# Optimization experiments

Hardware: AMD Instinct MI355X
Metric: run time of the kernel (lower is better)

## Reference

```python
import jax, jax.numpy as jnp
import numpy as np
from jax import lax

DIM = 512
NUM_HEADS = 8
RANK = 4
SR = 2
LN_EPS = 1e-5


def setup_inputs() -> dict:
    key = jax.random.key(0)
    ks = jax.random.split(key, 16)
    B, N, C = 8, 1024, DIM
    H = W = 32
    r = C // RANK  # 128 low-rank bottleneck
    std = 0.02
    x = jax.random.normal(ks[0], (B, N, C), dtype=jnp.float32)
    # training-path random mask: rand > sparsity(=0.5), True = masked out
    mask = jax.random.bernoulli(ks[1], 0.5, (B, NUM_HEADS, N, (H // SR) * (W // SR)))
    # low-rank QKV projection weights, torch Linear layout (out, in), no bias
    q_w1 = jax.random.normal(ks[2], (r, C), dtype=jnp.float32) * std
    q_w2 = jax.random.normal(ks[3], (C, r), dtype=jnp.float32) * std
    k_w1 = jax.random.normal(ks[4], (r, C), dtype=jnp.float32) * std
    k_w2 = jax.random.normal(ks[5], (C, r), dtype=jnp.float32) * std
    v_w1 = jax.random.normal(ks[6], (r, C), dtype=jnp.float32) * std
    v_w2 = jax.random.normal(ks[7], (C, r), dtype=jnp.float32) * std
    # depthwise sr conv: torch Conv2d(dim, dim, k=SR, stride=SR, groups=dim) -> (C,1,SR,SR)
    fan_out = SR * SR * C // C  # = SR*SR
    sr_w = jax.random.normal(ks[8], (C, 1, SR, SR), dtype=jnp.float32) * np.sqrt(2.0 / fan_out)
    sr_b = jnp.zeros((C,), dtype=jnp.float32)
    ln_g = jnp.ones((C,), dtype=jnp.float32)
    ln_b = jnp.zeros((C,), dtype=jnp.float32)
    proj_w = jax.random.normal(ks[9], (C, C), dtype=jnp.float32) * std
    proj_b = jnp.zeros((C,), dtype=jnp.float32)
    return {"x": x, "mask": mask, "q_w1": q_w1, "q_w2": q_w2, "k_w1": k_w1,
            "k_w2": k_w2, "v_w1": v_w1, "v_w2": v_w2, "sr_w": sr_w, "sr_b": sr_b,
            "ln_g": ln_g, "ln_b": ln_b, "proj_w": proj_w, "proj_b": proj_b,
            "H": H, "W": W}


def reference(x, mask, q_w1, q_w2, k_w1, k_w2, v_w1, v_w2, sr_w, sr_b,
              ln_g, ln_b, proj_w, proj_b, H, W):
    B, N, C = x.shape
    hd = C // NUM_HEADS
    scale = hd ** -0.5
    # low-rank q projection
    q = (x @ q_w1.T) @ q_w2.T  # (B,N,C)
    q = q.reshape(B, N, NUM_HEADS, hd).transpose(0, 2, 1, 3)  # (B,h,N,d)
    # spatial reduction: depthwise conv k=stride=SR, then LayerNorm
    x_ = x.transpose(0, 2, 1).reshape(B, C, H, W)
    x_ = lax.conv_general_dilated(x_, sr_w, (SR, SR), 'VALID',
                                  feature_group_count=C,
                                  dimension_numbers=('NCHW', 'OIHW', 'NCHW'))
    x_ = x_ + sr_b[None, :, None, None]
    x_ = x_.reshape(B, C, -1).transpose(0, 2, 1)  # (B, N_new, C)
    mu = jnp.mean(x_, axis=-1, keepdims=True)
    var = jnp.mean(jnp.square(x_ - mu), axis=-1, keepdims=True)
    x_ = (x_ - mu) / jnp.sqrt(var + LN_EPS) * ln_g + ln_b
    Nn = x_.shape[1]
    k = ((x_ @ k_w1.T) @ k_w2.T).reshape(B, Nn, NUM_HEADS, hd).transpose(0, 2, 1, 3)
    v = ((x_ @ v_w1.T) @ v_w2.T).reshape(B, Nn, NUM_HEADS, hd).transpose(0, 2, 1, 3)
    # masked scaled dot-product attention (training path: random mask -> -inf)
    attn = jnp.einsum('bhnd,bhmd->bhnm', q, k) * scale
    attn = jnp.where(mask, -jnp.inf, attn)
    attn = jax.nn.softmax(attn, axis=-1)
    out = jnp.einsum('bhnm,bhmd->bhnd', attn, v)  # (B,h,N,d)
    out = out.transpose(0, 2, 1, 3).reshape(B, N, C)
    out = out @ proj_w.T + proj_b
    return out
```

## Files before the change

kernel.cpp:

```cpp
#include <hip/hip_runtime.h>
#include <hip/hip_bf16.h>
#include <math.h>
#include <stdint.h>

#define DIMC   512
#define NHEAD  8
#define HD     64
#define NTOK   1024
#define MTOK   256
#define BSZ    8
#define LN_EPS 1e-5f

typedef __attribute__((ext_vector_type(8))) short  short8v;
typedef __attribute__((ext_vector_type(4))) float  f32x4;
typedef __attribute__((ext_vector_type(4))) unsigned short us4;

typedef const __attribute__((address_space(1))) unsigned int* gas1_t;
typedef __attribute__((address_space(3))) unsigned int*       las3_t;

__device__ __forceinline__ void gload_lds16(const void* g, void* l) {
    __builtin_amdgcn_global_load_lds((gas1_t)g, (las3_t)l, 16, 0, 0);
}

__device__ __forceinline__ unsigned short f2bf(float f) {
    union { float f; unsigned int u; } v; v.f = f;
    unsigned int u = v.u;
    return (unsigned short)((u + 0x7FFFu + ((u >> 16) & 1u)) >> 16);
}

__global__ void detect_mask_kernel(const unsigned int* __restrict__ m,
                                   int* __restrict__ flag)
{
    const int lane = threadIdx.x & 63;
    const unsigned int w = m[lane];
    const unsigned long long not01 = __ballot(w > 1u);
    const unsigned long long notf  = __ballot(w != 0u && w != 0x3F800000u);
    if (lane == 0) *flag = (not01 == 0ull) ? 0 : ((notf == 0ull) ? 2 : 1);
}

__global__ __launch_bounds__(256)
void pack_mask_kernel(const void* __restrict__ maskp, const int* __restrict__ flag,
                      unsigned long long* __restrict__ packed)
{
    const int w = threadIdx.x >> 6, lane = threadIdx.x & 63;
    const long long row = (long long)blockIdx.x * 4 + w;
    const int mtype = *flag;
    int m0, m1, m2, m3;
    if (mtype == 0) {
        const int4 v = ((const int4*)maskp)[row * 64 + lane];
        m0 = v.x; m1 = v.y; m2 = v.z; m3 = v.w;
    } else if (mtype == 1) {
        const uchar4 v = ((const uchar4*)maskp)[row * 64 + lane];
        m0 = v.x; m1 = v.y; m2 = v.z; m3 = v.w;
    } else {
        const float4 v = ((const float4*)maskp)[row * 64 + lane];
        m0 = (v.x != 0.f); m1 = (v.y != 0.f); m2 = (v.z != 0.f); m3 = (v.w != 0.f);
    }
    const unsigned long long b0 = __ballot(m0 != 0);
    const unsigned long long b1 = __ballot(m1 != 0);
    const unsigned long long b2 = __ballot(m2 != 0);
    const unsigned long long b3 = __ballot(m3 != 0);
    if (lane < 4) {
        const unsigned long long v = lane == 0 ? b0 : lane == 1 ? b1
                                   : lane == 2 ? b2 : b3;
        packed[row * 4 + lane] = v;
    }
}

__global__ __launch_bounds__(256)
void f32_to_bf16_kernel(const float* __restrict__ in, unsigned short* __restrict__ out,
                        int n4)
{
    for (int i = blockIdx.x * 256 + threadIdx.x; i < n4; i += gridDim.x * 256) {
        const float4 v = ((const float4*)in)[i];
        us4 p;
        p[0] = f2bf(v.x); p[1] = f2bf(v.y); p[2] = f2bf(v.z); p[3] = f2bf(v.w);
        ((us4*)out)[i] = p;
    }
}

__global__ __launch_bounds__(256)
void convert_weights_kernel(const float* __restrict__ qw1, const float* __restrict__ kw1,
                            const float* __restrict__ vw1, const float* __restrict__ qw2,
                            const float* __restrict__ kw2, const float* __restrict__ vw2,
                            const float* __restrict__ pw,  unsigned short* __restrict__ out,
                            unsigned short* __restrict__ w1t)
{
    const int e = (blockIdx.x * 256 + threadIdx.x) * 4;
    const float* src; int off;
    if      (e < 65536)  { src = qw1; off = e; }
    else if (e < 131072) { src = kw1; off = e - 65536; }
    else if (e < 196608) { src = vw1; off = e - 131072; }
    else if (e < 262144) { src = qw2; off = e - 196608; }
    else if (e < 327680) { src = kw2; off = e - 262144; }
    else if (e < 393216) { src = vw2; off = e - 327680; }
    else                 { src = pw;  off = e - 393216; }
    const float4 v = *(const float4*)(src + off);
    us4 p;
    p[0] = f2bf(v.x); p[1] = f2bf(v.y); p[2] = f2bf(v.z); p[3] = f2bf(v.w);
    *(us4*)(out + e) = p;
    if (e < 196608) {
        const int mat = e >> 16, rem = e & 65535;
        const int k = rem >> 9, j = rem & 511;
#pragma unroll
        for (int t = 0; t < 4; ++t)
            w1t[mat * 65536 + (j + t) * 128 + k] = p[t];
    }
}

template<int OUT_MODE, int BSEL>
__global__ __launch_bounds__(256)
void gemm_bf16(const unsigned short* __restrict__ A,
               const unsigned short* __restrict__ B,
               const float* __restrict__ bias,
               void* __restrict__ Cp, int M, int N, int K)
{
    __shared__ unsigned short As[2][128 * 64];
    __shared__ unsigned short Bs[2][128 * 64];

    const int tid  = threadIdx.x;
    const int w    = tid >> 6;
    const int lane = tid & 63;
    const int c16  = lane & 15;
    const int g    = lane >> 4;
    const int wr   = w >> 1, wc = w & 1;
    const size_t bm = (size_t)blockIdx.y * 128;
    const size_t bn = (size_t)blockIdx.x * 128;
    if (BSEL) B += (bm >> 9) * 65536;

    f32x4 acc[4][4];
#pragma unroll
    for (int i = 0; i < 4; ++i)
#pragma unroll
        for (int j = 0; j < 4; ++j) acc[i][j] = (f32x4){0.f, 0.f, 0.f, 0.f};

    const int NT = K >> 6;

    auto stage = [&](int buf, int kt) {
#pragma unroll
        for (int i = 0; i < 4; ++i) {
            const int o   = (((i * 4 + w) * 64) + lane) * 16;
            const int row = o >> 7;
            const int col = (o & 127) >> 1;
            gload_lds16(A + (bm + row) * K + kt + col, (char*)As[buf] + o);
        }
#pragma unroll
        for (int i = 0; i < 4; ++i) {
            const int o   = (((i * 4 + w) * 64) + lane) * 16;
            const int row = o >> 7;
            const int col = (o & 127) >> 1;
            gload_lds16(B + (bn + row) * K + kt + col, (char*)Bs[buf] + o);
        }
    };

    stage(0, 0);
    int cur = 0;
    for (int t = 0; t < NT; ++t) {
        if (t + 1 < NT) {
            stage(cur ^ 1, (t + 1) * 64);
            asm volatile("s_waitcnt vmcnt(8)" ::: "memory");
        } else {
            asm volatile("s_waitcnt vmcnt(0)" ::: "memory");
        }
        asm volatile("s_barrier" ::: "memory");
#pragma unroll
        for (int kk = 0; kk < 2; ++kk) {
            short8v a[4], bb[4];
#pragma unroll
            for (int mf = 0; mf < 4; ++mf)
                a[mf] = *(const short8v*)(&As[cur][(wr * 64 + mf * 16 + c16) * 64 + kk * 32 + g * 8]);
#pragma unroll
            for (int nf = 0; nf < 4; ++nf)
                bb[nf] = *(const short8v*)(&Bs[cur][(wc * 64 + nf * 16 + c16) * 64 + kk * 32 + g * 8]);
#pragma unroll
            for (int mf = 0; mf < 4; ++mf)
#pragma unroll
                for (int nf = 0; nf < 4; ++nf)
                    acc[mf][nf] = __builtin_amdgcn_mfma_f32_16x16x32_bf16(a[mf], bb[nf], acc[mf][nf], 0, 0, 0);
        }
        asm volatile("s_barrier" ::: "memory");
        cur ^= 1;
    }

#pragma unroll
    for (int mf = 0; mf < 4; ++mf) {
#pragma unroll
        for (int nf = 0; nf < 4; ++nf) {
            const size_t col = bn + wc * 64 + nf * 16 + c16;
            const size_t r0  = bm + wr * 64 + mf * 16 + g * 4;
            if (OUT_MODE == 0) {
                float* C = (float*)Cp;
                const float bv = (bias != nullptr) ? bias[col] : 0.f;
#pragma unroll
                for (int r = 0; r < 4; ++r)
                    C[(r0 + r) * N + col] = acc[mf][nf][r] + bv;
            } else if (OUT_MODE == 1) {
                unsigned short* C = (unsigned short*)Cp;
#pragma unroll
                for (int r = 0; r < 4; ++r)
                    C[(r0 + r) * N + col] = f2bf(acc[mf][nf][r]);
            } else {
                if (col < 512) {
                    unsigned short* Ck = (unsigned short*)Cp;
#pragma unroll
                    for (int r = 0; r < 4; ++r)
                        Ck[(r0 + r) * 512 + col] = f2bf(acc[mf][nf][r]);
                } else {
                    unsigned short* Cv = (unsigned short*)Cp + 1048576;
                    const size_t b  = r0 >> 8;
                    const size_t m0 = r0 & 255;
                    us4 p;
                    p[0] = f2bf(acc[mf][nf][0]); p[1] = f2bf(acc[mf][nf][1]);
                    p[2] = f2bf(acc[mf][nf][2]); p[3] = f2bf(acc[mf][nf][3]);
                    *(us4*)(Cv + (b * 512 + (col - 512)) * 256 + m0) = p;
                }
            }
        }
    }
}

__global__ __launch_bounds__(512)
void conv_ln_kernel(const float* __restrict__ x, const float* __restrict__ srw,
                    const float* __restrict__ srb, const float* __restrict__ lng,
                    const float* __restrict__ lnb, unsigned short* __restrict__ xr)
{
    const int c  = threadIdx.x;
    const int bn = blockIdx.x;
    const int b  = bn >> 8;
    const int np = bn & 255;
    const int ho = np >> 4, wo = np & 15;
    const int n00 = (ho * 2) * 32 + wo * 2;

    const float* xb = x + ((size_t)b * NTOK) * DIMC + c;
    const float4 w = *(const float4*)(srw + c * 4);
    float y = srb[c]
            + xb[(size_t)(n00     ) * DIMC] * w.x
            + xb[(size_t)(n00 + 1 ) * DIMC] * w.y
            + xb[(size_t)(n00 + 32) * DIMC] * w.z
            + xb[(size_t)(n00 + 33) * DIMC] * w.w;

    float s = y, s2 = y * y;
#pragma unroll
    for (int off = 32; off > 0; off >>= 1) {
        s  += __shfl_down(s,  off);
        s2 += __shfl_down(s2, off);
    }
    __shared__ float red[16];
    __shared__ float stats[2];
    const int lane = c & 63, wid = c >> 6;
    if (lane == 0) { red[wid] = s; red[8 + wid] = s2; }
    __syncthreads();
    if (c == 0) {
        float ts = 0.f, ts2 = 0.f;
#pragma unroll
        for (int i = 0; i < 8; ++i) { ts += red[i]; ts2 += red[8 + i]; }
        const float mu  = ts * (1.f / 512.f);
        const float var = ts2 * (1.f / 512.f) - mu * mu;
        stats[0] = mu;
        stats[1] = rsqrtf(var + LN_EPS);
    }
    __syncthreads();
    const float mu = stats[0], rstd = stats[1];
    xr[((size_t)(b * MTOK + np)) * DIMC + c] = f2bf((y - mu) * rstd * lng[c] + lnb[c]);
}

__global__ __launch_bounds__(256, 4)
void attn_mfma(const unsigned short* __restrict__ qb,
               const unsigned short* __restrict__ kb,
               const unsigned short* __restrict__ vt,
               const unsigned long long* __restrict__ pmask,
               unsigned short* __restrict__ ob)
{
    __shared__ unsigned short Ks[16384];

    const int tid  = threadIdx.x;
    const int w    = tid >> 6;
    const int lane = tid & 63;
    const int g    = lane >> 4;
    const int c16  = lane & 15;
    const int bh   = blockIdx.x & 63;
    const int qt   = blockIdx.x >> 6;
    const int b    = bh >> 3;
    const int h    = bh & 7;
    const int q0   = qt * 64 + w * 16;

    const unsigned short* kgb = kb + ((size_t)b * MTOK) * DIMC + h * HD;
#pragma unroll
    for (int t = 0; t < 8; ++t) {
        const int chunk = t * 256 + w * 64 + lane;
        const int o_dma = chunk * 16;
        const int row   = o_dma >> 7;
        const int o_log = o_dma ^ ((row & 7) << 4);
        const int slot  = (o_log >> 4) & 7;
        gload_lds16(kgb + (size_t)row * DIMC + slot * 8, (char*)Ks + o_dma);
    }

    const size_t prow = (size_t)bh * NTOK + q0 + g * 4;
    unsigned mlo[4], mhi[4];
#pragma unroll
    for (int r = 0; r < 4; ++r) {
        const unsigned long long pm = pmask[(prow + r) * 4 + (c16 & 3)] >> (c16 >> 2);
        mlo[r] = (unsigned)pm;
        mhi[r] = (unsigned)(pm >> 32);
    }
    short8v qf[2];
#pragma unroll
    for (int ks = 0; ks < 2; ++ks)
        qf[ks] = *(const short8v*)(qb + ((size_t)(b * NTOK + q0 + c16)) * DIMC
                                      + h * HD + ks * 32 + g * 8);

    asm volatile("s_waitcnt vmcnt(0)" ::: "memory");
    asm volatile("s_barrier" ::: "memory");

    f32x4 s[16];
#pragma unroll
    for (int nf = 0; nf < 16; ++nf) s[nf] = (f32x4){0.f, 0.f, 0.f, 0.f};
#pragma unroll
    for (int nf = 0; nf < 16; ++nf) {
        const int kr = nf * 16 + c16;
        const int sw = (kr & 7) << 4;
#pragma unroll
        for (int ks = 0; ks < 2; ++ks) {
            const int o = (kr << 7) + ks * 64 + g * 16;
            const short8v kf = *(const short8v*)((const char*)Ks + (o ^ sw));
            s[nf] = __builtin_amdgcn_mfma_f32_16x16x32_bf16(qf[ks], kf, s[nf], 0, 0, 0);
        }
    }

    const float scale = 0.125f;
#pragma unroll
    for (int nf = 0; nf < 16; ++nf) {
#pragma unroll
        for (int r = 0; r < 4; ++r) {
            const unsigned bit = ((nf < 8 ? (mlo[r] >> (nf * 4))
                                          : (mhi[r] >> ((nf - 8) * 4))) & 1u);
            s[nf][r] = bit ? -INFINITY : s[nf][r] * scale;
        }
    }

    float mx[4] = {-1e30f, -1e30f, -1e30f, -1e30f};
#pragma unroll
    for (int nf = 0; nf < 16; ++nf)
#pragma unroll
        for (int r = 0; r < 4; ++r) mx[r] = fmaxf(mx[r], s[nf][r]);
#pragma unroll
    for (int off = 8; off >= 1; off >>= 1)
#pragma unroll
        for (int r = 0; r < 4; ++r) mx[r] = fmaxf(mx[r], __shfl_xor(mx[r], off, 64));

    float sm[4] = {0.f, 0.f, 0.f, 0.f};
#pragma unroll
    for (int nf = 0; nf < 16; ++nf)
#pragma unroll
        for (int r = 0; r < 4; ++r) {
            const float p = __expf(s[nf][r] - mx[r]);
            s[nf][r] = p;
            sm[r] += p;
        }
#pragma unroll
    for (int off = 8; off >= 1; off >>= 1)
#pragma unroll
        for (int r = 0; r < 4; ++r) sm[r] += __shfl_xor(sm[r], off, 64);
    float inv[4];
#pragma unroll
    for (int r = 0; r < 4; ++r) inv[r] = 1.0f / sm[r];

    asm volatile("s_barrier" ::: "memory");

    unsigned short* pw = Ks + w * 4096;
#pragma unroll
    for (int nf = 0; nf < 16; ++nf) {
        const int key = nf * 16 + c16;
#pragma unroll
        for (int r = 0; r < 4; ++r) {
            const int row = g * 4 + r;
            pw[row * 256 + (key ^ ((row & 7) << 3))] = f2bf(s[nf][r] * inv[r]);
        }
    }

    f32x4 o[4];
#pragma unroll
    for (int df = 0; df < 4; ++df) o[df] = (f32x4){0.f, 0.f, 0.f, 0.f};

    const int prw = c16;
    const unsigned short* pr = pw + prw * 256;
#pragma unroll
    for (int kf = 0; kf < 8; ++kf) {
        const int k0 = kf * 32 + g * 8;
        const short8v pa = *(const short8v*)(pr + (k0 ^ ((prw & 7) << 3)));
#pragma unroll
        for (int df = 0; df < 4; ++df) {
            const short8v vf = *(const short8v*)(vt + ((size_t)(b * DIMC + h * HD + df * 16 + c16)) * MTOK + k0);
            o[df] = __builtin_amdgcn_mfma_f32_16x16x32_bf16(pa, vf, o[df], 0, 0, 0);
        }
    }

#pragma unroll
    for (int df = 0; df < 4; ++df)
#pragma unroll
        for (int r = 0; r < 4; ++r)
            ob[((size_t)(b * NTOK + q0 + g * 4 + r)) * DIMC + h * HD + df * 16 + c16] =
                f2bf(o[df][r]);
}

extern "C" void kernel_launch(void* const* d_in, const int* in_sizes, int n_in,
                              void* d_out, int out_size, void* d_ws, size_t ws_size,
                              hipStream_t stream)
{
    const float* x      = (const float*)d_in[0];
    const void*  mask   = d_in[1];
    const float* q_w1   = (const float*)d_in[2];
    const float* q_w2   = (const float*)d_in[3];
    const float* k_w1   = (const float*)d_in[4];
    const float* k_w2   = (const float*)d_in[5];
    const float* v_w1   = (const float*)d_in[6];
    const float* v_w2   = (const float*)d_in[7];
    const float* sr_w   = (const float*)d_in[8];
    const float* sr_b   = (const float*)d_in[9];
    const float* ln_g   = (const float*)d_in[10];
    const float* ln_b   = (const float*)d_in[11];
    const float* proj_w = (const float*)d_in[12];
    const float* proj_b = (const float*)d_in[13];

    unsigned char* wsb = (unsigned char*)d_ws;
    unsigned short* xb16 = (unsigned short*)(wsb + 0);
    unsigned short* ao16 = (unsigned short*)(wsb + 0);
    unsigned short* qb16 = (unsigned short*)(wsb + (8u  << 20));
    unsigned short* xrb  = (unsigned short*)(wsb + (16u << 20));
    unsigned short* w1t  = (unsigned short*)(wsb + (18u << 20));
    unsigned short* kb16 = (unsigned short*)(wsb + (19u << 20));
    unsigned short* vt16 = (unsigned short*)(wsb + (21u << 20));
    unsigned short* wts  = (unsigned short*)(wsb + (23u << 20));
    unsigned short* wc16 = (unsigned short*)(wsb + (25u << 20));
    unsigned long long* pmask = (unsigned long long*)(wsb + (27u << 20));
    int*            flag = (int*)(wsb + (29u << 20));

    const int QW2 = 196608, PW = 393216;

    detect_mask_kernel<<<1, 64, 0, stream>>>((const unsigned int*)mask, flag);
    pack_mask_kernel<<<16384, 256, 0, stream>>>(mask, flag, pmask);
    convert_weights_kernel<<<640, 256, 0, stream>>>(q_w1, k_w1, v_w1, q_w2, k_w2, v_w2,
                                                    proj_w, wts, w1t);
    f32_to_bf16_kernel<<<2048, 256, 0, stream>>>(x, xb16, 1048576);
    conv_ln_kernel<<<2048, 512, 0, stream>>>(x, sr_w, sr_b, ln_g, ln_b, xrb);

    gemm_bf16<1, 1><<<dim3(4, 12), 256, 0, stream>>>(wts + QW2, w1t, nullptr, wc16, 1536, 512, 128);

    gemm_bf16<1, 0><<<dim3(4, 64), 256, 0, stream>>>(xb16, wc16, nullptr, qb16, 8192, 512, 512);

    gemm_bf16<3, 0><<<dim3(8, 16), 256, 0, stream>>>(xrb, wc16 + 262144, nullptr, kb16, 2048, 1024, 512);

    attn_mfma<<<1024, 256, 0, stream>>>(qb16, kb16, vt16, pmask, ao16);

    gemm_bf16<0, 0><<<dim3(4, 64), 256, 0, stream>>>(ao16, wts + PW, proj_b, d_out, 8192, 512, 512);
}
```

Baseline: 220.6 us.

## Fuse x conversion into conv-LN, inline mask detection, retile GEMM with XCD remap

Removes the separate mask-detect and f32-to-bf16 kernels: mask type detection moves into the pack kernel, and the bf16 copy of x is written by the conv+LayerNorm kernel, which already reads x. The GEMM switches to 64x128 tiles on a 1D grid whose block index is remapped so neighbouring tiles land on the same XCD, which doubles the number of workgroups. Attention raises wave priority around its MFMA loops. The changes cut launches and a full pass over x, at the cost of less reuse per GEMM tile.

```diff
diff --git a/kernel.cpp b/kernel.cpp
--- a/kernel.cpp
+++ b/kernel.cpp
@@ -28,23 +28,17 @@
     return (unsigned short)((u + 0x7FFFu + ((u >> 16) & 1u)) >> 16);
 }
 
-__global__ void detect_mask_kernel(const unsigned int* __restrict__ m,
-                                   int* __restrict__ flag)
-{
-    const int lane = threadIdx.x & 63;
-    const unsigned int w = m[lane];
-    const unsigned long long not01 = __ballot(w > 1u);
-    const unsigned long long notf  = __ballot(w != 0u && w != 0x3F800000u);
-    if (lane == 0) *flag = (not01 == 0ull) ? 0 : ((notf == 0ull) ? 2 : 1);
-}
-
 __global__ __launch_bounds__(256)
-void pack_mask_kernel(const void* __restrict__ maskp, const int* __restrict__ flag,
+void pack_mask_kernel(const void* __restrict__ maskp,
                       unsigned long long* __restrict__ packed)
 {
     const int w = threadIdx.x >> 6, lane = threadIdx.x & 63;
+    const unsigned int pw_ = ((const unsigned int*)maskp)[lane];
+    const unsigned long long not01 = __ballot(pw_ > 1u);
+    const unsigned long long notf  = __ballot(pw_ != 0u && pw_ != 0x3F800000u);
+    const int mtype = (not01 == 0ull) ? 0 : ((notf == 0ull) ? 2 : 1);
+
     const long long row = (long long)blockIdx.x * 4 + w;
-    const int mtype = *flag;
     int m0, m1, m2, m3;
     if (mtype == 0) {
         const int4 v = ((const int4*)maskp)[row * 64 + lane];
@@ -64,18 +58,6 @@
         const unsigned long long v = lane == 0 ? b0 : lane == 1 ? b1
                                    : lane == 2 ? b2 : b3;
         packed[row * 4 + lane] = v;
-    }
-}
-
-__global__ __launch_bounds__(256)
-void f32_to_bf16_kernel(const float* __restrict__ in, unsigned short* __restrict__ out,
-                        int n4)
-{
-    for (int i = blockIdx.x * 256 + threadIdx.x; i < n4; i += gridDim.x * 256) {
-        const float4 v = ((const float4*)in)[i];
-        us4 p;
-        p[0] = f2bf(v.x); p[1] = f2bf(v.y); p[2] = f2bf(v.z); p[3] = f2bf(v.w);
-        ((us4*)out)[i] = p;
     }
 }
 
@@ -108,6 +90,58 @@
     }
 }
 
+__global__ __launch_bounds__(512)
+void prep_x_kernel(const float* __restrict__ x, const float* __restrict__ srw,
+                   const float* __restrict__ srb, const float* __restrict__ lng,
+                   const float* __restrict__ lnb, unsigned short* __restrict__ xb16,
+                   unsigned short* __restrict__ xr)
+{
+    const int c  = threadIdx.x;
+    const int bn = blockIdx.x;
+    const int b  = bn >> 8;
+    const int np = bn & 255;
+    const int ho = np >> 4, wo = np & 15;
+    const int n00 = (ho * 2) * 32 + wo * 2;
+
+    const size_t base = ((size_t)b * NTOK) * DIMC + c;
+    const float x0 = x[base + (size_t)(n00     ) * DIMC];
+    const float x1 = x[base + (size_t)(n00 + 1 ) * DIMC];
+    const float x2 = x[base + (size_t)(n00 + 32) * DIMC];
+    const float x3 = x[base + (size_t)(n00 + 33) * DIMC];
+
+    xb16[base + (size_t)(n00     ) * DIMC] = f2bf(x0);
+    xb16[base + (size_t)(n00 + 1 ) * DIMC] = f2bf(x1);
+    xb16[base + (size_t)(n00 + 32) * DIMC] = f2bf(x2);
+    xb16[base + (size_t)(n00 + 33) * DIMC] = f2bf(x3);
+
+    const float4 w = *(const float4*)(srw + c * 4);
+    float y = srb[c] + x0 * w.x + x1 * w.y + x2 * w.z + x3 * w.w;
+
+    float s = y, s2 = y * y;
+#pragma unroll
+    for (int off = 32; off > 0; off >>= 1) {
+        s  += __shfl_down(s,  off);
+        s2 += __shfl_down(s2, off);
+    }
+    __shared__ float red[16];
+    __shared__ float stats[2];
+    const int lane = c & 63, wid = c >> 6;
+    if (lane == 0) { red[wid] = s; red[8 + wid] = s2; }
+    __syncthreads();
+    if (c == 0) {
+        float ts = 0.f, ts2 = 0.f;
+#pragma unroll
+        for (int i = 0; i < 8; ++i) { ts += red[i]; ts2 += red[8 + i]; }
+        const float mu  = ts * (1.f / 512.f);
+        const float var = ts2 * (1.f / 512.f) - mu * mu;
+        stats[0] = mu;
+        stats[1] = rsqrtf(var + LN_EPS);
+    }
+    __syncthreads();
+    const float mu = stats[0], rstd = stats[1];
+    xr[((size_t)(b * MTOK + np)) * DIMC + c] = f2bf((y - mu) * rstd * lng[c] + lnb[c]);
+}
+
 template<int OUT_MODE, int BSEL>
 __global__ __launch_bounds__(256)
 void gemm_bf16(const unsigned short* __restrict__ A,
@@ -115,7 +149,7 @@
                const float* __restrict__ bias,
                void* __restrict__ Cp, int M, int N, int K)
 {
-    __shared__ unsigned short As[2][128 * 64];
+    __shared__ unsigned short As[2][64 * 64];
     __shared__ unsigned short Bs[2][128 * 64];
 
     const int tid  = threadIdx.x;
@@ -124,13 +158,17 @@
     const int c16  = lane & 15;
     const int g    = lane >> 4;
     const int wr   = w >> 1, wc = w & 1;
-    const size_t bm = (size_t)blockIdx.y * 128;
-    const size_t bn = (size_t)blockIdx.x * 128;
+
+    const int nwg = gridDim.x;
+    const int L   = ((int)blockIdx.x & 7) * (nwg >> 3) + ((int)blockIdx.x >> 3);
+    const int gx  = N >> 7;
+    const size_t bm = (size_t)(L / gx) * 64;
+    const size_t bn = (size_t)(L % gx) * 128;
     if (BSEL) B += (bm >> 9) * 65536;
 
-    f32x4 acc[4][4];
-#pragma unroll
-    for (int i = 0; i < 4; ++i)
+    f32x4 acc[2][4];
+#pragma unroll
+    for (int i = 0; i < 2; ++i)
 #pragma unroll
         for (int j = 0; j < 4; ++j) acc[i][j] = (f32x4){0.f, 0.f, 0.f, 0.f};
 
@@ -138,15 +176,15 @@
 
     auto stage = [&](int buf, int kt) {
 #pragma unroll
-        for (int i = 0; i < 4; ++i) {
-            const int o   = (((i * 4 + w) * 64) + lane) * 16;
+        for (int i = 0; i < 2; ++i) {
+            const int o   = (tid + i * 256) * 16;
             const int row = o >> 7;
             const int col = (o & 127) >> 1;
             gload_lds16(A + (bm + row) * K + kt + col, (char*)As[buf] + o);
         }
 #pragma unroll
         for (int i = 0; i < 4; ++i) {
-            const int o   = (((i * 4 + w) * 64) + lane) * 16;
+            const int o   = (tid + i * 256) * 16;
             const int row = o >> 7;
             const int col = (o & 127) >> 1;
             gload_lds16(B + (bn + row) * K + kt + col, (char*)Bs[buf] + o);
@@ -158,22 +196,22 @@
     for (int t = 0; t < NT; ++t) {
         if (t + 1 < NT) {
             stage(cur ^ 1, (t + 1) * 64);
-            asm volatile("s_waitcnt vmcnt(8)" ::: "memory");
+            asm volatile("s_waitcnt vmcnt(6)" ::: "memory");
         } else {
             asm volatile("s_waitcnt vmcnt(0)" ::: "memory");
         }
         asm volatile("s_barrier" ::: "memory");
 #pragma unroll
         for (int kk = 0; kk < 2; ++kk) {
-            short8v a[4], bb[4];
-#pragma unroll
-            for (int mf = 0; mf < 4; ++mf)
-                a[mf] = *(const short8v*)(&As[cur][(wr * 64 + mf * 16 + c16) * 64 + kk * 32 + g * 8]);
+            short8v a[2], bb[4];
+#pragma unroll
+            for (int mf = 0; mf < 2; ++mf)
+                a[mf] = *(const short8v*)(&As[cur][(wr * 32 + mf * 16 + c16) * 64 + kk * 32 + g * 8]);
 #pragma unroll
             for (int nf = 0; nf < 4; ++nf)
                 bb[nf] = *(const short8v*)(&Bs[cur][(wc * 64 + nf * 16 + c16) * 64 + kk * 32 + g * 8]);
 #pragma unroll
-            for (int mf = 0; mf < 4; ++mf)
+            for (int mf = 0; mf < 2; ++mf)
 #pragma unroll
                 for (int nf = 0; nf < 4; ++nf)
                     acc[mf][nf] = __builtin_amdgcn_mfma_f32_16x16x32_bf16(a[mf], bb[nf], acc[mf][nf], 0, 0, 0);
@@ -183,11 +221,11 @@
     }
 
 #pragma unroll
-    for (int mf = 0; mf < 4; ++mf) {
+    for (int mf = 0; mf < 2; ++mf) {
 #pragma unroll
         for (int nf = 0; nf < 4; ++nf) {
             const size_t col = bn + wc * 64 + nf * 16 + c16;
-            const size_t r0  = bm + wr * 64 + mf * 16 + g * 4;
+            const size_t r0  = bm + wr * 32 + mf * 16 + g * 4;
             if (OUT_MODE == 0) {
                 float* C = (float*)Cp;
                 const float bv = (bias != nullptr) ? bias[col] : 0.f;
@@ -219,51 +257,6 @@
     }
 }
 
-__global__ __launch_bounds__(512)
-void conv_ln_kernel(const float* __restrict__ x, const float* __restrict__ srw,
-                    const float* __restrict__ srb, const float* __restrict__ lng,
-                    const float* __restrict__ lnb, unsigned short* __restrict__ xr)
-{
-    const int c  = threadIdx.x;
-    const int bn = blockIdx.x;
-    const int b  = bn >> 8;
-    const int np = bn & 255;
-    const int ho = np >> 4, wo = np & 15;
-    const int n00 = (ho * 2) * 32 + wo * 2;
-
-    const float* xb = x + ((size_t)b * NTOK) * DIMC + c;
-    const float4 w = *(const float4*)(srw + c * 4);
-    float y = srb[c]
-            + xb[(size_t)(n00     ) * DIMC] * w.x
-            + xb[(size_t)(n00 + 1 ) * DIMC] * w.y
-            + xb[(size_t)(n00 + 32) * DIMC] * w.z
-            + xb[(size_t)(n00 + 33) * DIMC] * w.w;
-
-    float s = y, s2 = y * y;
-#pragma unroll
-    for (int off = 32; off > 0; off >>= 1) {
-        s  += __shfl_down(s,  off);
-        s2 += __shfl_down(s2, off);
-    }
-    __shared__ float red[16];
-    __shared__ float stats[2];
-    const int lane = c & 63, wid = c >> 6;
-    if (lane == 0) { red[wid] = s; red[8 + wid] = s2; }
-    __syncthreads();
-    if (c == 0) {
-        float ts = 0.f, ts2 = 0.f;
-#pragma unroll
-        for (int i = 0; i < 8; ++i) { ts += red[i]; ts2 += red[8 + i]; }
-        const float mu  = ts * (1.f / 512.f);
-        const float var = ts2 * (1.f / 512.f) - mu * mu;
-        stats[0] = mu;
-        stats[1] = rsqrtf(var + LN_EPS);
-    }
-    __syncthreads();
-    const float mu = stats[0], rstd = stats[1];
-    xr[((size_t)(b * MTOK + np)) * DIMC + c] = f2bf((y - mu) * rstd * lng[c] + lnb[c]);
-}
-
 __global__ __launch_bounds__(256, 4)
 void attn_mfma(const unsigned short* __restrict__ qb,
                const unsigned short* __restrict__ kb,
@@ -315,6 +308,7 @@
     f32x4 s[16];
 #pragma unroll
     for (int nf = 0; nf < 16; ++nf) s[nf] = (f32x4){0.f, 0.f, 0.f, 0.f};
+    __builtin_amdgcn_s_setprio(1);
 #pragma unroll
     for (int nf = 0; nf < 16; ++nf) {
         const int kr = nf * 16 + c16;
@@ -326,6 +320,7 @@
             s[nf] = __builtin_amdgcn_mfma_f32_16x16x32_bf16(qf[ks], kf, s[nf], 0, 0, 0);
         }
     }
+    __builtin_amdgcn_s_setprio(0);
 
     const float scale = 0.125f;
 #pragma unroll
@@ -384,6 +379,7 @@
 
     const int prw = c16;
     const unsigned short* pr = pw + prw * 256;
+    __builtin_amdgcn_s_setprio(1);
 #pragma unroll
     for (int kf = 0; kf < 8; ++kf) {
         const int k0 = kf * 32 + g * 8;
@@ -394,6 +390,7 @@
             o[df] = __builtin_amdgcn_mfma_f32_16x16x32_bf16(pa, vf, o[df], 0, 0, 0);
         }
     }
+    __builtin_amdgcn_s_setprio(0);
 
 #pragma unroll
     for (int df = 0; df < 4; ++df)
@@ -433,24 +430,21 @@
     unsigned short* wts  = (unsigned short*)(wsb + (23u << 20));
     unsigned short* wc16 = (unsigned short*)(wsb + (25u << 20));
     unsigned long long* pmask = (unsigned long long*)(wsb + (27u << 20));
-    int*            flag = (int*)(wsb + (29u << 20));
 
     const int QW2 = 196608, PW = 393216;
 
-    detect_mask_kernel<<<1, 64, 0, stream>>>((const unsigned int*)mask, flag);
-    pack_mask_kernel<<<16384, 256, 0, stream>>>(mask, flag, pmask);
+    pack_mask_kernel<<<16384, 256, 0, stream>>>(mask, pmask);
     convert_weights_kernel<<<640, 256, 0, stream>>>(q_w1, k_w1, v_w1, q_w2, k_w2, v_w2,
                                                     proj_w, wts, w1t);
-    f32_to_bf16_kernel<<<2048, 256, 0, stream>>>(x, xb16, 1048576);
-    conv_ln_kernel<<<2048, 512, 0, stream>>>(x, sr_w, sr_b, ln_g, ln_b, xrb);
-
-    gemm_bf16<1, 1><<<dim3(4, 12), 256, 0, stream>>>(wts + QW2, w1t, nullptr, wc16, 1536, 512, 128);
-
-    gemm_bf16<1, 0><<<dim3(4, 64), 256, 0, stream>>>(xb16, wc16, nullptr, qb16, 8192, 512, 512);
-
-    gemm_bf16<3, 0><<<dim3(8, 16), 256, 0, stream>>>(xrb, wc16 + 262144, nullptr, kb16, 2048, 1024, 512);
+    prep_x_kernel<<<2048, 512, 0, stream>>>(x, sr_w, sr_b, ln_g, ln_b, xb16, xrb);
+
+    gemm_bf16<1, 1><<<96, 256, 0, stream>>>(wts + QW2, w1t, nullptr, wc16, 1536, 512, 128);
+
+    gemm_bf16<1, 0><<<512, 256, 0, stream>>>(xb16, wc16, nullptr, qb16, 8192, 512, 512);
+
+    gemm_bf16<3, 0><<<256, 256, 0, stream>>>(xrb, wc16 + 262144, nullptr, kb16, 2048, 1024, 512);
 
     attn_mfma<<<1024, 256, 0, stream>>>(qb16, kb16, vt16, pmask, ao16);
 
-    gemm_bf16<0, 0><<<dim3(4, 64), 256, 0, stream>>>(ao16, wts + PW, proj_b, d_out, 8192, 512, 512);
-}
+    gemm_bf16<0, 0><<<512, 256, 0, stream>>>(ao16, wts + PW, proj_b, d_out, 8192, 512, 512);
+}
```

Result: faster. 207.6 us (-5.9%).
